# Performance work log

Measured on AMD Instinct MI355X. Metric: run time of the kernel, lower is better.

## Reference

```python
import jax, jax.numpy as jnp
import numpy as np

HEADS = 8

def setup_inputs() -> dict:
    key = jax.random.key(0)
    ks = jax.random.split(key, 4)
    b, n, d = 4, 4097, 128  # n = 64*64 + 1 (CLS + spatial)
    x = jax.random.normal(ks[0], (b, n, d), dtype=jnp.float32)
    W_qkv = jax.random.normal(ks[1], (d, 3 * d), dtype=jnp.float32) * (d ** -0.5)
    b_qkv = jnp.zeros((3 * d,), dtype=jnp.float32)
    W_out = jax.random.normal(ks[2], (d, d), dtype=jnp.float32) * (d ** -0.5)
    b_out = jnp.zeros((d,), dtype=jnp.float32)
    return {"x": x, "W_qkv": W_qkv, "b_qkv": b_qkv, "W_out": W_out, "b_out": b_out}

def reference(x, W_qkv, b_qkv, W_out, b_out):
    b, n, d = x.shape
    h = HEADS
    dh = d // h
    scale = d ** -0.5  # note: module scales by dim**-0.5, not head_dim**-0.5
    qkv = x @ W_qkv + b_qkv                      # [b, n, 3d]
    q, k, v = jnp.split(qkv, 3, axis=-1)
    def to_heads(t):
        return t.reshape(b, n, h, dh).transpose(0, 2, 1, 3)  # [b, h, n, dh]
    q, k, v = to_heads(q), to_heads(k), to_heads(v)
    dots = jnp.einsum('bhid,bhjd->bhij', q, k) * scale       # [b, h, n, n]
    attn = jax.nn.softmax(dots, axis=-1)
    out = jnp.einsum('bhij,bhjd->bhid', attn, v)             # [b, h, n, dh]
    out = out.transpose(0, 2, 1, 3).reshape(b, n, d)
    return out @ W_out + b_out
```

## Files before the change

kernel.cpp:

```cpp
#include <hip/hip_runtime.h>
#include <hip/hip_bf16.h>
#include <stdint.h>


#define BB 4
#define NN 4097
#define NNP 4112
#define DD 128
#define HH 8
#define DH 16
#define BH (BB*HH)
#define ROWS (BB*NN)
#define MT  1025

typedef _Float16 h4 __attribute__((ext_vector_type(4)));
typedef _Float16 h8 __attribute__((ext_vector_type(8)));
typedef __fp16   fp16v2 __attribute__((ext_vector_type(2)));
typedef float    f4 __attribute__((ext_vector_type(4)));

#define QSCALE (0.08838834764831845f * 1.4426950408889634f)

#if __has_builtin(__builtin_amdgcn_exp2f)
#define EXP2F(x) __builtin_amdgcn_exp2f(x)
#else
#define EXP2F(x) exp2f(x)
#endif

union H4u { h4 v; fp16v2 p[2]; };

static __device__ __forceinline__ H4u pack4u(float a, float b, float c, float d) {
    H4u u;
#if __has_builtin(__builtin_amdgcn_cvt_pkrtz)
    u.p[0] = __builtin_amdgcn_cvt_pkrtz(a, b);
    u.p[1] = __builtin_amdgcn_cvt_pkrtz(c, d);
#else
    u.v[0] = (_Float16)a; u.v[1] = (_Float16)b; u.v[2] = (_Float16)c; u.v[3] = (_Float16)d;
#endif
    return u;
}

__global__ __launch_bounds__(256) void prep(
    const float* __restrict__ x,
    const float* __restrict__ Wqkv,
    const float* __restrict__ Wout,
    _Float16* __restrict__ x16,
    _Float16* __restrict__ WqkvT,
    _Float16* __restrict__ WoutT)
{
    const int id = blockIdx.x*256 + threadIdx.x;
    const int NX8 = ROWS*DD/8;
    if (id < NX8) {
        const float4* s = (const float4*)(x + (size_t)id*8);
        const float4 a = s[0], b = s[1];
        const H4u u0 = pack4u(a.x, a.y, a.z, a.w);
        const H4u u1 = pack4u(b.x, b.y, b.z, b.w);
        h4* d = (h4*)(x16 + (size_t)id*8);
        d[0] = u0.v; d[1] = u1.v;
    } else if (id < NX8 + 384*128) {
        const int e = id - NX8;
        const int n = e >> 7, k = e & 127;
        const float s = (n < 128) ? QSCALE : 1.0f;
        WqkvT[e] = (_Float16)(Wqkv[k*384 + n] * s);
    } else if (id < NX8 + 384*128 + 128*128) {
        const int e = id - NX8 - 384*128;
        const int n = e >> 7, k = e & 127;
        WoutT[e] = (_Float16)(Wout[k*128 + n]);
    }
}

__global__ __launch_bounds__(256) void qkv_mfma(
    const _Float16* __restrict__ x16,
    const _Float16* __restrict__ WqkvT,
    const float* __restrict__ bqkv,
    _Float16* __restrict__ Qh,
    _Float16* __restrict__ Kh,
    _Float16* __restrict__ Vh)
{
    const int wid  = blockIdx.x*4 + (threadIdx.x >> 6);
    if (wid >= MT) return;
    const int lane = threadIdx.x & 63;
    const int quad = lane >> 4, l16 = lane & 15;

    const int arow = wid*16 + l16;
    const int arc  = (arow < ROWS) ? arow : (ROWS - 1);
    h4 af[8];
    #pragma unroll
    for (int kk = 0; kk < 8; ++kk)
        af[kk] = *(const h4*)(x16 + (size_t)arc*DD + kk*16 + quad*4);

    const int r0 = wid*16 + quad*4;

    for (int nt = 0; nt < 24; nt += 2) {
        const float b0 = bqkv[nt*16 + l16]      * ((nt   < 8) ? QSCALE : 1.0f);
        const float b1 = bqkv[nt*16 + 16 + l16] * ((nt+1 < 8) ? QSCALE : 1.0f);
        f4 a0 = {b0,b0,b0,b0}, a1 = {b1,b1,b1,b1};
        #pragma unroll
        for (int kk = 0; kk < 8; ++kk) {
            const h4 bf0 = *(const h4*)(WqkvT + (size_t)(nt*16     + l16)*DD + kk*16 + quad*4);
            const h4 bf1 = *(const h4*)(WqkvT + (size_t)(nt*16 + 16 + l16)*DD + kk*16 + quad*4);
            a0 = __builtin_amdgcn_mfma_f32_16x16x16f16(af[kk], bf0, a0, 0, 0, 0);
            a1 = __builtin_amdgcn_mfma_f32_16x16x16f16(af[kk], bf1, a1, 0, 0, 0);
        }
        #pragma unroll
        for (int u = 0; u < 2; ++u) {
            const int ntc = nt + u;
            const int which = ntc >> 3, head = ntc & 7;
            _Float16* base = (which == 0) ? Qh : ((which == 1) ? Kh : Vh);
            const f4 av = u ? a1 : a0;
            #pragma unroll
            for (int r = 0; r < 4; ++r) {
                const int row = r0 + r;
                if (row < ROWS) {
                    const int bidx = row / NN;
                    const int nrow = row - bidx*NN;
                    base[((size_t)(bidx*HH + head)*NNP + nrow)*DH + l16] = (_Float16)av[r];
                }
            }
        }
    }
}

__global__ __launch_bounds__(256) void vt_transpose(
    const _Float16* __restrict__ Vh,
    _Float16* __restrict__ Vt)
{
    __shared__ _Float16 tile[128][DH + 2];
    const int tl  = blockIdx.x;
    const int bh  = blockIdx.y;
    const int tid = threadIdx.x;
    const int n0  = tl * 128;
    const int rem = (n0 + 128 <= NNP) ? 128 : (NNP - n0);

    {
        const int r  = tid >> 1;
        const int i8 = (tid & 1) * 8;
        const int rc = (r < rem) ? r : (rem - 1);
        const h8 v = *(const h8*)(Vh + ((size_t)bh*NNP + n0 + rc)*DH + i8);
        #pragma unroll
        for (int j = 0; j < 8; ++j) tile[r][i8 + j] = v[j];
    }
    __syncthreads();
    {
        const int i    = tid >> 4;
        const int nseg = tid & 15;
        if (nseg * 8 < rem) {
            h8 v;
            #pragma unroll
            for (int j = 0; j < 8; ++j) v[j] = tile[nseg*8 + j][i];
            *(h8*)(Vt + ((size_t)bh*DH + i)*NNP + n0 + nseg*8) = v;
        }
    }
}

__global__ __launch_bounds__(256, 8) void attn_mfma(
    const _Float16* __restrict__ Qh,
    const _Float16* __restrict__ Kh,
    const _Float16* __restrict__ Vt,
    _Float16* __restrict__ PACC,
    float* __restrict__ PL)
{
    const int qt   = blockIdx.x;
    const int bh   = blockIdx.y;
    const int sp   = blockIdx.z;
    const int tid  = threadIdx.x;
    const int wave = tid >> 6;
    const int lane = tid & 63;
    const int quad = lane >> 4;
    const int l16  = lane & 15;
    const int bidx = bh >> 3, head = bh & 7;

    const int qbase = qt*256 + wave*64;

    const _Float16* Qb = Qh + (size_t)bh*NNP*DH;
    h4 qf[4];
    #pragma unroll
    for (int g = 0; g < 4; ++g) {
        const int qr = qbase + g*16 + l16;
        const int qc = (qr < NN) ? qr : (NN-1);
        qf[g] = *(const h4*)(Qb + (size_t)qc*DH + quad*4);
    }

    f4 acc[4] = {{0,0,0,0},{0,0,0,0},{0,0,0,0},{0,0,0,0}};
    float ls[4] = {0.f,0.f,0.f,0.f};

    const int t0 = sp*64;
    const int t1 = t0 + 64;

    const _Float16* kp = Kh + ((size_t)bh*NNP + (size_t)t0*16 + l16)*DH + quad*4;
    const _Float16* vp = Vt + ((size_t)bh*DH + l16)*NNP + t0*16 + quad*4;

    h4 ak = *(const h4*)kp;
    h4 av = *(const h4*)vp;
    const f4 zero = {0.f,0.f,0.f,0.f};
#if __has_builtin(__builtin_amdgcn_fdot2)
    const fp16v2 one2 = {(__fp16)1.0f, (__fp16)1.0f};
#endif

    for (int tt = t0; tt < t1; ++tt) {
        kp += 16*DH; vp += 16;
        const h4 nak = *(const h4*)kp;
        const h4 nav = *(const h4*)vp;
        #pragma unroll
        for (int g = 0; g < 4; ++g) {
            f4 d = __builtin_amdgcn_mfma_f32_16x16x16f16(ak, qf[g], zero, 0, 0, 0);
            const float p0 = EXP2F(d[0]), p1 = EXP2F(d[1]), p2 = EXP2F(d[2]), p3 = EXP2F(d[3]);
            const H4u pb = pack4u(p0, p1, p2, p3);
#if __has_builtin(__builtin_amdgcn_fdot2)
            ls[g] = __builtin_amdgcn_fdot2(pb.p[0], one2,
                     __builtin_amdgcn_fdot2(pb.p[1], one2, ls[g], false), false);
#else
            ls[g] += (p0 + p1) + (p2 + p3);
#endif
            acc[g] = __builtin_amdgcn_mfma_f32_16x16x16f16(av, pb.v, acc[g], 0, 0, 0);
        }
        ak = nak; av = nav;
    }

    if (sp == 3) {
        #pragma unroll
        for (int g = 0; g < 4; ++g) {
            f4 d = __builtin_amdgcn_mfma_f32_16x16x16f16(ak, qf[g], zero, 0, 0, 0);
            const float p0 = (quad == 0) ? EXP2F(d[0]) : 0.f;
            ls[g] += p0;
            const H4u pb = pack4u(p0, 0.f, 0.f, 0.f);
            acc[g] = __builtin_amdgcn_mfma_f32_16x16x16f16(av, pb.v, acc[g], 0, 0, 0);
        }
    }

    const size_t rb = (size_t)sp*ROWS + (size_t)bidx*NN;
    #pragma unroll
    for (int g = 0; g < 4; ++g) {
        float l = ls[g];
        l += __shfl_xor(l, 16);
        l += __shfl_xor(l, 32);
        const int qr = qbase + g*16 + l16;
        if (qr < NN) {
            const float inv = 1.0f / l;
            const H4u st = pack4u(acc[g][0]*inv, acc[g][1]*inv, acc[g][2]*inv, acc[g][3]*inv);
            *(h4*)(PACC + (rb + qr)*DD + head*DH + quad*4) = st.v;
            if (quad == 0) PL[(rb + qr)*HH + head] = l;
        }
    }
}

__global__ __launch_bounds__(256) void out_mfma(
    const _Float16* __restrict__ PACC,
    const float* __restrict__ PL,
    const _Float16* __restrict__ WoutT,
    const float* __restrict__ bout,
    float* __restrict__ out)
{
    const int wid  = blockIdx.x*4 + (threadIdx.x >> 6);
    if (wid >= MT) return;
    const int lane = threadIdx.x & 63;
    const int quad = lane >> 4, l16 = lane & 15;

    const int arow = wid*16 + l16;
    const int arc  = (arow < ROWS) ? arow : (ROWS - 1);

    h4 af[8];
    #pragma unroll
    for (int kk = 0; kk < 8; ++kk) {
        float n0 = 0.f, n1 = 0.f, n2 = 0.f, n3 = 0.f, lsum = 0.f;
        #pragma unroll
        for (int sp = 0; sp < 4; ++sp) {
            const float l = PL[((size_t)sp*ROWS + arc)*HH + kk];
            lsum += l;
            const h4 p = *(const h4*)(PACC + ((size_t)sp*ROWS + arc)*DD + kk*16 + quad*4);
            n0 += l*(float)p[0]; n1 += l*(float)p[1];
            n2 += l*(float)p[2]; n3 += l*(float)p[3];
        }
        const float inv = 1.0f / lsum;
        const H4u u = pack4u(n0*inv, n1*inv, n2*inv, n3*inv);
        af[kk] = u.v;
    }

    const int r0 = wid*16 + quad*4;

    for (int nt = 0; nt < 8; nt += 2) {
        const float b0 = bout[nt*16 + l16];
        const float b1 = bout[nt*16 + 16 + l16];
        f4 a0 = {b0,b0,b0,b0}, a1 = {b1,b1,b1,b1};
        #pragma unroll
        for (int kk = 0; kk < 8; ++kk) {
            const h4 bf0 = *(const h4*)(WoutT + (size_t)(nt*16      + l16)*DD + kk*16 + quad*4);
            const h4 bf1 = *(const h4*)(WoutT + (size_t)(nt*16 + 16 + l16)*DD + kk*16 + quad*4);
            a0 = __builtin_amdgcn_mfma_f32_16x16x16f16(af[kk], bf0, a0, 0, 0, 0);
            a1 = __builtin_amdgcn_mfma_f32_16x16x16f16(af[kk], bf1, a1, 0, 0, 0);
        }
        #pragma unroll
        for (int r = 0; r < 4; ++r) {
            const int row = r0 + r;
            if (row < ROWS) {
                out[(size_t)row*DD + nt*16      + l16] = a0[r];
                out[(size_t)row*DD + nt*16 + 16 + l16] = a1[r];
            }
        }
    }
}

extern "C" void kernel_launch(void* const* d_in, const int* in_sizes, int n_in,
                              void* d_out, int out_size, void* d_ws, size_t ws_size,
                              hipStream_t stream) {
    const float* x    = (const float*)d_in[0];
    const float* Wqkv = (const float*)d_in[1];
    const float* bqkv = (const float*)d_in[2];
    const float* Wout = (const float*)d_in[3];
    const float* bout = (const float*)d_in[4];
    for (int i = 0; i < n_in; ++i) {
        switch (in_sizes[i]) {
            case 2097664: x    = (const float*)d_in[i]; break;
            case 49152:   Wqkv = (const float*)d_in[i]; break;
            case 384:     bqkv = (const float*)d_in[i]; break;
            case 16384:   Wout = (const float*)d_in[i]; break;
            case 128:     bout = (const float*)d_in[i]; break;
            default: break;
        }
    }
    float* out = (float*)d_out;

    const size_t perh = (size_t)BH * NNP * DH;
    _Float16* Qh   = (_Float16*)d_ws;
    _Float16* Kh   = Qh + perh;
    _Float16* Vt   = Kh + perh;
    _Float16* Vh   = Vt + perh;
    _Float16* PACC = Vh;
    _Float16* x16  = Vh + perh;
    float*    PL    = (float*)(PACC + (size_t)4*ROWS*DD);
    _Float16* WqkvT = (_Float16*)(PL + (size_t)4*ROWS*HH);
    _Float16* WoutT = WqkvT + 384*128;

    const int NX8 = ROWS*DD/8;
    const int prep_total = NX8 + 384*128 + 128*128;

    hipLaunchKernelGGL(prep, dim3((prep_total + 255)/256), dim3(256), 0, stream,
                       x, Wqkv, Wout, x16, WqkvT, WoutT);
    hipLaunchKernelGGL(qkv_mfma, dim3((MT + 3)/4), dim3(256), 0, stream,
                       x16, WqkvT, bqkv, Qh, Kh, Vh);
    hipLaunchKernelGGL(vt_transpose, dim3(33, BH), dim3(256), 0, stream,
                       Vh, Vt);
    hipLaunchKernelGGL(attn_mfma, dim3(17, BH, 4), dim3(256), 0, stream,
                       Qh, Kh, Vt, PACC, PL);
    hipLaunchKernelGGL(out_mfma, dim3((MT + 3)/4), dim3(256), 0, stream,
                       PACC, PL, WoutT, bout, out);
}
```

Before: 196.8 us.

## Switch MFMA to 16x16x32 f16 and re-split QKV and attention work

Replaces the 16x16x16 f16 MFMA with the 16x16x32 variant in the QKV projection, the output projection and the QK^T step of attention. In attention the head dim of 16 is zero-padded in the Q operand so the K=32 instruction still computes the same dot. The QKV kernel now gives each 256-thread block one 16-row tile with four waves splitting the 24 output column tiles. Attention blocks shrink to 128 threads with a doubled grid and a new launch bound. The padded QK^T wastes half of each MFMA, and the smaller blocks change occupancy and scheduling.

```diff
diff --git a/kernel.cpp b/kernel.cpp
--- a/kernel.cpp
+++ b/kernel.cpp
@@ -27,6 +27,7 @@
 #endif
 
 union H4u { h4 v; fp16v2 p[2]; };
+union H8u { h8 v; fp16v2 p[4]; };
 
 static __device__ __forceinline__ H4u pack4u(float a, float b, float c, float d) {
     H4u u;
@@ -76,30 +77,31 @@
     _Float16* __restrict__ Kh,
     _Float16* __restrict__ Vh)
 {
-    const int wid  = blockIdx.x*4 + (threadIdx.x >> 6);
-    if (wid >= MT) return;
+    const int wid  = blockIdx.x;
+    const int wave = threadIdx.x >> 6;
     const int lane = threadIdx.x & 63;
     const int quad = lane >> 4, l16 = lane & 15;
 
     const int arow = wid*16 + l16;
     const int arc  = (arow < ROWS) ? arow : (ROWS - 1);
-    h4 af[8];
+    h8 af[4];
     #pragma unroll
-    for (int kk = 0; kk < 8; ++kk)
-        af[kk] = *(const h4*)(x16 + (size_t)arc*DD + kk*16 + quad*4);
+    for (int kk = 0; kk < 4; ++kk)
+        af[kk] = *(const h8*)(x16 + (size_t)arc*DD + kk*32 + quad*8);
 
     const int r0 = wid*16 + quad*4;
-
-    for (int nt = 0; nt < 24; nt += 2) {
+    const int nt0 = wave*6;
+
+    for (int nt = nt0; nt < nt0 + 6; nt += 2) {
         const float b0 = bqkv[nt*16 + l16]      * ((nt   < 8) ? QSCALE : 1.0f);
         const float b1 = bqkv[nt*16 + 16 + l16] * ((nt+1 < 8) ? QSCALE : 1.0f);
         f4 a0 = {b0,b0,b0,b0}, a1 = {b1,b1,b1,b1};
         #pragma unroll
-        for (int kk = 0; kk < 8; ++kk) {
-            const h4 bf0 = *(const h4*)(WqkvT + (size_t)(nt*16     + l16)*DD + kk*16 + quad*4);
-            const h4 bf1 = *(const h4*)(WqkvT + (size_t)(nt*16 + 16 + l16)*DD + kk*16 + quad*4);
-            a0 = __builtin_amdgcn_mfma_f32_16x16x16f16(af[kk], bf0, a0, 0, 0, 0);
-            a1 = __builtin_amdgcn_mfma_f32_16x16x16f16(af[kk], bf1, a1, 0, 0, 0);
+        for (int kk = 0; kk < 4; ++kk) {
+            const h8 bf0 = *(const h8*)(WqkvT + (size_t)(nt*16      + l16)*DD + kk*32 + quad*8);
+            const h8 bf1 = *(const h8*)(WqkvT + (size_t)(nt*16 + 16 + l16)*DD + kk*32 + quad*8);
+            a0 = __builtin_amdgcn_mfma_f32_16x16x32_f16(af[kk], bf0, a0, 0, 0, 0);
+            a1 = __builtin_amdgcn_mfma_f32_16x16x32_f16(af[kk], bf1, a1, 0, 0, 0);
         }
         #pragma unroll
         for (int u = 0; u < 2; ++u) {
@@ -152,14 +154,14 @@
     }
 }
 
-__global__ __launch_bounds__(256, 8) void attn_mfma(
+__global__ __launch_bounds__(128, 6) void attn_mfma(
     const _Float16* __restrict__ Qh,
     const _Float16* __restrict__ Kh,
     const _Float16* __restrict__ Vt,
     _Float16* __restrict__ PACC,
     float* __restrict__ PL)
 {
-    const int qt   = blockIdx.x;
+    const int qc2  = blockIdx.x;
     const int bh   = blockIdx.y;
     const int sp   = blockIdx.z;
     const int tid  = threadIdx.x;
@@ -169,15 +171,19 @@
     const int l16  = lane & 15;
     const int bidx = bh >> 3, head = bh & 7;
 
-    const int qbase = qt*256 + wave*64;
+    const int qbase = (qc2*2 + wave)*64;
 
     const _Float16* Qb = Qh + (size_t)bh*NNP*DH;
-    h4 qf[4];
+    h8 qf[4];
     #pragma unroll
     for (int g = 0; g < 4; ++g) {
-        const int qr = qbase + g*16 + l16;
-        const int qc = (qr < NN) ? qr : (NN-1);
-        qf[g] = *(const h4*)(Qb + (size_t)qc*DH + quad*4);
+        h8 t = {0,0,0,0,0,0,0,0};
+        if (quad < 2) {
+            const int qr = qbase + g*16 + l16;
+            const int qc = (qr < NN) ? qr : (NN-1);
+            t = *(const h8*)(Qb + (size_t)qc*DH + quad*8);
+        }
+        qf[g] = t;
     }
 
     f4 acc[4] = {{0,0,0,0},{0,0,0,0},{0,0,0,0},{0,0,0,0}};
@@ -186,10 +192,10 @@
     const int t0 = sp*64;
     const int t1 = t0 + 64;
 
-    const _Float16* kp = Kh + ((size_t)bh*NNP + (size_t)t0*16 + l16)*DH + quad*4;
+    const _Float16* kp = Kh + ((size_t)bh*NNP + (size_t)t0*16 + l16)*DH + (quad&1)*8;
     const _Float16* vp = Vt + ((size_t)bh*DH + l16)*NNP + t0*16 + quad*4;
 
-    h4 ak = *(const h4*)kp;
+    h8 ak = *(const h8*)kp;
     h4 av = *(const h4*)vp;
     const f4 zero = {0.f,0.f,0.f,0.f};
 #if __has_builtin(__builtin_amdgcn_fdot2)
@@ -198,11 +204,11 @@
 
     for (int tt = t0; tt < t1; ++tt) {
         kp += 16*DH; vp += 16;
-        const h4 nak = *(const h4*)kp;
+        const h8 nak = *(const h8*)kp;
         const h4 nav = *(const h4*)vp;
         #pragma unroll
         for (int g = 0; g < 4; ++g) {
-            f4 d = __builtin_amdgcn_mfma_f32_16x16x16f16(ak, qf[g], zero, 0, 0, 0);
+            f4 d = __builtin_amdgcn_mfma_f32_16x16x32_f16(ak, qf[g], zero, 0, 0, 0);
             const float p0 = EXP2F(d[0]), p1 = EXP2F(d[1]), p2 = EXP2F(d[2]), p3 = EXP2F(d[3]);
             const H4u pb = pack4u(p0, p1, p2, p3);
 #if __has_builtin(__builtin_amdgcn_fdot2)
@@ -219,7 +225,7 @@
     if (sp == 3) {
         #pragma unroll
         for (int g = 0; g < 4; ++g) {
-            f4 d = __builtin_amdgcn_mfma_f32_16x16x16f16(ak, qf[g], zero, 0, 0, 0);
+            f4 d = __builtin_amdgcn_mfma_f32_16x16x32_f16(ak, qf[g], zero, 0, 0, 0);
             const float p0 = (quad == 0) ? EXP2F(d[0]) : 0.f;
             ls[g] += p0;
             const H4u pb = pack4u(p0, 0.f, 0.f, 0.f);
@@ -254,24 +260,39 @@
     if (wid >= MT) return;
     const int lane = threadIdx.x & 63;
     const int quad = lane >> 4, l16 = lane & 15;
+    const int hq   = quad >> 1;
 
     const int arow = wid*16 + l16;
     const int arc  = (arow < ROWS) ? arow : (ROWS - 1);
 
-    h4 af[8];
+    h8 af[4];
     #pragma unroll
-    for (int kk = 0; kk < 8; ++kk) {
-        float n0 = 0.f, n1 = 0.f, n2 = 0.f, n3 = 0.f, lsum = 0.f;
+    for (int kk = 0; kk < 4; ++kk) {
+        const int head = kk*2 + hq;
+        float n0=0.f,n1=0.f,n2=0.f,n3=0.f,n4=0.f,n5=0.f,n6=0.f,n7=0.f,lsum=0.f;
         #pragma unroll
         for (int sp = 0; sp < 4; ++sp) {
-            const float l = PL[((size_t)sp*ROWS + arc)*HH + kk];
+            const float l = PL[((size_t)sp*ROWS + arc)*HH + head];
             lsum += l;
-            const h4 p = *(const h4*)(PACC + ((size_t)sp*ROWS + arc)*DD + kk*16 + quad*4);
+            const h8 p = *(const h8*)(PACC + ((size_t)sp*ROWS + arc)*DD + kk*32 + quad*8);
             n0 += l*(float)p[0]; n1 += l*(float)p[1];
             n2 += l*(float)p[2]; n3 += l*(float)p[3];
+            n4 += l*(float)p[4]; n5 += l*(float)p[5];
+            n6 += l*(float)p[6]; n7 += l*(float)p[7];
         }
         const float inv = 1.0f / lsum;
-        const H4u u = pack4u(n0*inv, n1*inv, n2*inv, n3*inv);
+        H8u u;
+#if __has_builtin(__builtin_amdgcn_cvt_pkrtz)
+        u.p[0] = __builtin_amdgcn_cvt_pkrtz(n0*inv, n1*inv);
+        u.p[1] = __builtin_amdgcn_cvt_pkrtz(n2*inv, n3*inv);
+        u.p[2] = __builtin_amdgcn_cvt_pkrtz(n4*inv, n5*inv);
+        u.p[3] = __builtin_amdgcn_cvt_pkrtz(n6*inv, n7*inv);
+#else
+        u.v[0]=(_Float16)(n0*inv); u.v[1]=(_Float16)(n1*inv);
+        u.v[2]=(_Float16)(n2*inv); u.v[3]=(_Float16)(n3*inv);
+        u.v[4]=(_Float16)(n4*inv); u.v[5]=(_Float16)(n5*inv);
+        u.v[6]=(_Float16)(n6*inv); u.v[7]=(_Float16)(n7*inv);
+#endif
         af[kk] = u.v;
     }
 
@@ -282,11 +303,11 @@
         const float b1 = bout[nt*16 + 16 + l16];
         f4 a0 = {b0,b0,b0,b0}, a1 = {b1,b1,b1,b1};
         #pragma unroll
-        for (int kk = 0; kk < 8; ++kk) {
-            const h4 bf0 = *(const h4*)(WoutT + (size_t)(nt*16      + l16)*DD + kk*16 + quad*4);
-            const h4 bf1 = *(const h4*)(WoutT + (size_t)(nt*16 + 16 + l16)*DD + kk*16 + quad*4);
-            a0 = __builtin_amdgcn_mfma_f32_16x16x16f16(af[kk], bf0, a0, 0, 0, 0);
-            a1 = __builtin_amdgcn_mfma_f32_16x16x16f16(af[kk], bf1, a1, 0, 0, 0);
+        for (int kk = 0; kk < 4; ++kk) {
+            const h8 bf0 = *(const h8*)(WoutT + (size_t)(nt*16      + l16)*DD + kk*32 + quad*8);
+            const h8 bf1 = *(const h8*)(WoutT + (size_t)(nt*16 + 16 + l16)*DD + kk*32 + quad*8);
+            a0 = __builtin_amdgcn_mfma_f32_16x16x32_f16(af[kk], bf0, a0, 0, 0, 0);
+            a1 = __builtin_amdgcn_mfma_f32_16x16x32_f16(af[kk], bf1, a1, 0, 0, 0);
         }
         #pragma unroll
         for (int r = 0; r < 4; ++r) {
@@ -335,11 +356,11 @@
 
     hipLaunchKernelGGL(prep, dim3((prep_total + 255)/256), dim3(256), 0, stream,
                        x, Wqkv, Wout, x16, WqkvT, WoutT);
-    hipLaunchKernelGGL(qkv_mfma, dim3((MT + 3)/4), dim3(256), 0, stream,
+    hipLaunchKernelGGL(qkv_mfma, dim3(MT), dim3(256), 0, stream,
                        x16, WqkvT, bqkv, Qh, Kh, Vh);
     hipLaunchKernelGGL(vt_transpose, dim3(33, BH), dim3(256), 0, stream,
                        Vh, Vt);
-    hipLaunchKernelGGL(attn_mfma, dim3(17, BH, 4), dim3(256), 0, stream,
+    hipLaunchKernelGGL(attn_mfma, dim3(33, BH, 4), dim3(128), 0, stream,
                        Qh, Kh, Vt, PACC, PL);
     hipLaunchKernelGGL(out_mfma, dim3((MT + 3)/4), dim3(256), 0, stream,
                        PACC, PL, WoutT, bout, out);
```

New measurement: 188.2 us. -4.4%, faster.
